# Kernel tuning notes

Measured on AMD Instinct MI355X. Metric: run time of the kernel, lower is better.

The kernel has to match this reference:

```python
import jax, jax.numpy as jnp
import numpy as np

N_NODES = 100000
N_EDGES = 3200000
D_IN = 128
D_HID = 128
N_CLASSES = 2
N_GRAPHS = 64


def _gcn_conv(x, src, dst, norm, W, b, n_nodes):
    # GCNConv: x' = D^-1/2 (A+I) D^-1/2 (x W) + b  (self-loops already in src/dst)
    h = x @ W                                   # [N, out]
    msg = h[src] * norm[:, None]                # gather + per-edge scale [E', out]
    agg = jax.ops.segment_sum(msg, dst, num_segments=n_nodes)  # scatter-add
    return agg + b


def setup_inputs() -> dict:
    key = jax.random.key(0)
    ks = jax.random.split(key, 10)
    x = jax.random.normal(ks[0], (N_NODES, D_IN), dtype=jnp.float32)
    edge_index = jax.random.randint(ks[1], (2, N_EDGES), 0, N_NODES, dtype=jnp.int32)
    batch = jnp.sort(jax.random.randint(ks[2], (N_NODES,), 0, N_GRAPHS, dtype=jnp.int32))
    s1 = 1.0 / np.sqrt(D_IN)
    s2 = 1.0 / np.sqrt(D_HID)
    W1 = jax.random.uniform(ks[3], (D_IN, D_HID), jnp.float32, -s1, s1)
    b1 = jnp.zeros((D_HID,), jnp.float32)
    W2 = jax.random.uniform(ks[4], (D_HID, D_HID), jnp.float32, -s2, s2)
    b2 = jnp.zeros((D_HID,), jnp.float32)
    Wc = jax.random.uniform(ks[5], (D_HID, N_CLASSES), jnp.float32, -s2, s2)
    bc = jnp.zeros((N_CLASSES,), jnp.float32)
    return {"x": x, "edge_index": edge_index, "batch": batch,
            "W1": W1, "b1": b1, "W2": W2, "b2": b2, "Wc": Wc, "bc": bc,
            "num_graphs": N_GRAPHS}


def reference(x, edge_index, batch, W1, b1, W2, b2, Wc, bc, num_graphs):
    n = x.shape[0]
    loops = jnp.arange(n, dtype=edge_index.dtype)
    src = jnp.concatenate([edge_index[0], loops])
    dst = jnp.concatenate([edge_index[1], loops])
    # symmetric normalization with self-loops (degree over destinations, as PyG)
    deg = jax.ops.segment_sum(jnp.ones_like(dst, dtype=x.dtype), dst, num_segments=n)
    dinv = jnp.where(deg > 0, jax.lax.rsqrt(jnp.maximum(deg, 1.0)), 0.0)
    norm = dinv[src] * dinv[dst]                # [E']

    h = _gcn_conv(x, src, dst, norm, W1, b1, n)
    h = jax.nn.relu(h)                          # dropout is identity at eval
    h = _gcn_conv(h, src, dst, norm, W2, b2, n)

    # global_mean_pool over graph ids
    sums = jax.ops.segment_sum(h, batch, num_segments=num_graphs)      # [G, H]
    cnts = jax.ops.segment_sum(jnp.ones((n,), h.dtype), batch, num_segments=num_graphs)
    pooled = sums / jnp.maximum(cnts, 1.0)[:, None]

    return pooled @ Wc + bc                     # [G, num_classes]
```

## Files before the change

### kernel.cpp

```cpp
#include <hip/hip_runtime.h>
#include <hip/hip_bf16.h>

#define D 128
#define NGRAPH 64
#define POOLBLK 256
#define PBCHUNK 4096
#define WINSZ 256
#define WINSLOTS 16384
#define XP 136

typedef __attribute__((ext_vector_type(4))) float f32x4;
typedef __attribute__((ext_vector_type(8))) short bf16x8;

__device__ __forceinline__ unsigned short f2bf(float f) {
    union { float f; unsigned int i; } u; u.f = f;
    unsigned int r = u.i + 0x7fffu + ((u.i >> 16) & 1u);
    return (unsigned short)(r >> 16);
}
__device__ __forceinline__ float2 bf2_to_f2(unsigned int u) {
    union { unsigned int i; float f; } a, b;
    a.i = u << 16;
    b.i = u & 0xffff0000u;
    return make_float2(a.f, b.f);
}


__global__ __launch_bounds__(256) void k_prep(const float* __restrict__ W2,
                                              const float* __restrict__ Wc,
                                              const float* __restrict__ b2,
                                              const float* __restrict__ bc,
                                              float* __restrict__ Weff,
                                              float* __restrict__ beff,
                                              int* __restrict__ zero_region,
                                              int zero_words) {
    int t = threadIdx.x;
    int i = t >> 1, c = t & 1;
    float acc = 0.f;
    for (int k = 0; k < D; ++k) acc += W2[i * D + k] * Wc[k * 2 + c];
    Weff[i * 2 + c] = acc;
    if (i == 0) {
        float s = 0.f;
        for (int k = 0; k < D; ++k) s += b2[k] * Wc[k * 2 + c];
        beff[c] = s + bc[c];
    }
    for (int j = t; j < zero_words; j += 256) zero_region[j] = 0;
}


__global__ __launch_bounds__(256) void k_part(const int* __restrict__ src,
                                              const int* __restrict__ dst,
                                              int* __restrict__ cursor,
                                              unsigned* __restrict__ ebuf,
                                              int E, int nb) {
    __shared__ unsigned spack[PBCHUNK];
    __shared__ unsigned short sbin[PBCHUNK];
    __shared__ unsigned short slrank[PBCHUNK];
    __shared__ int hist[400];
    __shared__ int base[400];
    int tid = threadIdx.x;
    for (int i = tid; i < nb; i += 256) hist[i] = 0;
    __syncthreads();
    int b0 = blockIdx.x * PBCHUNK;
    int cnt = min(PBCHUNK, E - b0);
    for (int j = tid; j < cnt; j += 256) {
        int s = __builtin_nontemporal_load(&src[b0 + j]);
        int d = __builtin_nontemporal_load(&dst[b0 + j]);
        int bin = d >> 8;
        spack[j] = (unsigned)s | ((unsigned)(d & 255) << 17);
        sbin[j] = (unsigned short)bin;
        slrank[j] = (unsigned short)atomicAdd(&hist[bin], 1);
    }
    __syncthreads();
    for (int i = tid; i < nb; i += 256)
        base[i] = hist[i] ? atomicAdd(&cursor[i], hist[i]) : 0;
    __syncthreads();
    for (int j = tid; j < cnt; j += 256) {
        int bin = sbin[j];
        ebuf[(size_t)bin * WINSLOTS + base[bin] + slrank[j]] = spack[j];
    }
}

__global__ __launch_bounds__(256) void k_csrwin(const unsigned* __restrict__ ebuf,
                                                const int* __restrict__ cursor,
                                                int* __restrict__ csr,
                                                int2* __restrict__ offcnt,
                                                float* __restrict__ dinv, int n) {
    __shared__ int hist[WINSZ];
    __shared__ int lscan[WINSZ];
    __shared__ int sexcl[WINSZ];
    int b = blockIdx.x;
    int tid = threadIdx.x;
    hist[tid] = 0;
    __syncthreads();
    int cnt = cursor[b];
    const unsigned* eb = ebuf + (size_t)b * WINSLOTS;
    for (int j = tid; j < cnt; j += 256)
        atomicAdd(&hist[eb[j] >> 17], 1);
    __syncthreads();
    int deg = hist[tid];
    lscan[tid] = deg;
    __syncthreads();
    for (int off = 1; off < 256; off <<= 1) {
        int y = (tid >= off) ? lscan[tid - off] : 0;
        __syncthreads();
        lscan[tid] += y;
        __syncthreads();
    }
    int excl = lscan[tid] - deg;
    int v = b * WINSZ + tid;
    int gbase = b * WINSLOTS;
    if (v < n) {
        offcnt[v] = make_int2(gbase + excl, deg);
        dinv[v] = rsqrtf((float)(deg + 1));
    }
    hist[tid] = 0;
    sexcl[tid] = excl;
    __syncthreads();
    for (int j = tid; j < cnt; j += 256) {
        unsigned p = eb[j];
        int d8 = (int)(p >> 17);
        int lr = atomicAdd(&hist[d8], 1);
        csr[gbase + sexcl[d8] + lr] = (int)(p & 0x1FFFFu);
    }
}


__global__ __launch_bounds__(256) void k_gemm_mfma(const float* __restrict__ X,
                                                   const float* __restrict__ W1,
                                                   unsigned short* __restrict__ H, int nrows) {
    __shared__ unsigned short xs[64][XP];
    __shared__ unsigned short wt[128][XP];
    int tid = threadIdx.x;
    int m0 = blockIdx.x * 64;
    for (int i = tid; i < 2048; i += 256) {
        int elt = i * 8;
        int k = elt >> 7, n0 = elt & 127;
        float4 a = *(const float4*)&W1[k * D + n0];
        float4 b = *(const float4*)&W1[k * D + n0 + 4];
        wt[n0 + 0][k] = f2bf(a.x); wt[n0 + 1][k] = f2bf(a.y);
        wt[n0 + 2][k] = f2bf(a.z); wt[n0 + 3][k] = f2bf(a.w);
        wt[n0 + 4][k] = f2bf(b.x); wt[n0 + 5][k] = f2bf(b.y);
        wt[n0 + 6][k] = f2bf(b.z); wt[n0 + 7][k] = f2bf(b.w);
    }
    for (int i = tid; i < 2048; i += 256) {
        int elt = i * 4;
        int r = elt >> 7, c = elt & 127;
        int gr = m0 + r;
        float4 v = (gr < nrows) ? *(const float4*)&X[(size_t)gr * D + c]
                                : make_float4(0.f, 0.f, 0.f, 0.f);
        ushort4 bv;
        bv.x = f2bf(v.x); bv.y = f2bf(v.y); bv.z = f2bf(v.z); bv.w = f2bf(v.w);
        *(ushort4*)&xs[r][c] = bv;
    }
    __syncthreads();
    int wv = tid >> 6, lane = tid & 63;
    int lrow = lane & 15, lk = (lane >> 4) * 8;
    f32x4 acc[8];
#pragma unroll
    for (int i = 0; i < 8; ++i) acc[i] = (f32x4){0.f, 0.f, 0.f, 0.f};
#pragma unroll
    for (int kk = 0; kk < 128; kk += 32) {
        bf16x8 a = *(bf16x8*)&xs[wv * 16 + lrow][kk + lk];
#pragma unroll
        for (int nt = 0; nt < 8; ++nt) {
            bf16x8 b = *(bf16x8*)&wt[nt * 16 + lrow][kk + lk];
            acc[nt] = __builtin_amdgcn_mfma_f32_16x16x32_bf16(a, b, acc[nt], 0, 0, 0);
        }
    }
    int orow = m0 + wv * 16 + (lane >> 4) * 4;
#pragma unroll
    for (int nt = 0; nt < 8; ++nt) {
#pragma unroll
        for (int r = 0; r < 4; ++r) {
            int gr = orow + r;
            if (gr < nrows) H[(size_t)gr * D + nt * 16 + lrow] = f2bf(acc[nt][r]);
        }
    }
}


__global__ __launch_bounds__(256) void k_agg_proj(const unsigned short* __restrict__ H,
                                                  const int2* __restrict__ offcnt,
                                                  const int* __restrict__ csr,
                                                  const float* __restrict__ dinv,
                                                  const float* __restrict__ bias,
                                                  const float* __restrict__ Weff,
                                                  float2* __restrict__ z, int n) {
    int wid = threadIdx.x >> 6;
    int lane = threadIdx.x & 63;
    int v = blockIdx.x * 4 + wid;
    if (v >= n) return;
    float dv = dinv[v];
    int l2 = lane * 2;
    unsigned us = *(const unsigned*)(H + (size_t)v * D + l2);
    float2 hs = bf2_to_f2(us);
    float dv2 = dv * dv;
    float2 acc = make_float2(hs.x * dv2, hs.y * dv2);
    int2 oc = offcnt[v];
    int e = oc.x, eE = oc.x + oc.y;
    for (; e + 7 < eE; e += 8) {
        int s[8];
#pragma unroll
        for (int j = 0; j < 8; ++j) s[j] = csr[e + j];
        unsigned u[8];
#pragma unroll
        for (int j = 0; j < 8; ++j) u[j] = *(const unsigned*)(H + (size_t)s[j] * D + l2);
        float w[8];
#pragma unroll
        for (int j = 0; j < 8; ++j) w[j] = dinv[s[j]] * dv;
#pragma unroll
        for (int j = 0; j < 8; ++j) {
            float2 h = bf2_to_f2(u[j]);
            acc.x += h.x * w[j]; acc.y += h.y * w[j];
        }
    }
    for (; e + 3 < eE; e += 4) {
        int s0 = csr[e], s1 = csr[e + 1], s2 = csr[e + 2], s3 = csr[e + 3];
        unsigned u0 = *(const unsigned*)(H + (size_t)s0 * D + l2);
        unsigned u1 = *(const unsigned*)(H + (size_t)s1 * D + l2);
        unsigned u2 = *(const unsigned*)(H + (size_t)s2 * D + l2);
        unsigned u3 = *(const unsigned*)(H + (size_t)s3 * D + l2);
        float w0 = dinv[s0] * dv, w1 = dinv[s1] * dv;
        float w2 = dinv[s2] * dv, w3 = dinv[s3] * dv;
        float2 h0 = bf2_to_f2(u0), h1 = bf2_to_f2(u1);
        float2 h2 = bf2_to_f2(u2), h3 = bf2_to_f2(u3);
        acc.x += h0.x * w0; acc.y += h0.y * w0;
        acc.x += h1.x * w1; acc.y += h1.y * w1;
        acc.x += h2.x * w2; acc.y += h2.y * w2;
        acc.x += h3.x * w3; acc.y += h3.y * w3;
    }
    for (; e < eE; ++e) {
        int s0 = csr[e];
        float w0 = dinv[s0] * dv;
        unsigned u0 = *(const unsigned*)(H + (size_t)s0 * D + l2);
        float2 h0 = bf2_to_f2(u0);
        acc.x += h0.x * w0; acc.y += h0.y * w0;
    }
    float2 b = ((const float2*)bias)[lane];
    acc.x = fmaxf(acc.x + b.x, 0.f);
    acc.y = fmaxf(acc.y + b.y, 0.f);
    float4 wv = *(const float4*)&Weff[l2 * 2];
    float z0 = acc.x * wv.x + acc.y * wv.z;
    float z1 = acc.x * wv.y + acc.y * wv.w;
#pragma unroll
    for (int off = 32; off >= 1; off >>= 1) {
        z0 += __shfl_xor(z0, off, 64);
        z1 += __shfl_xor(z1, off, 64);
    }
    if (lane == 0) z[v] = make_float2(z0, z1);
}


__global__ __launch_bounds__(256) void k_pool_edges(const float2* __restrict__ z,
                                                    const int* __restrict__ src,
                                                    const int* __restrict__ dst,
                                                    const float* __restrict__ dinv,
                                                    const int* __restrict__ batch,
                                                    float* __restrict__ tsum,
                                                    int* __restrict__ cnt,
                                                    int n, int E) {
    __shared__ float t[4][NGRAPH * 2];
    __shared__ int scnt[4][NGRAPH];
    int tid = threadIdx.x;
    int wv = tid >> 6;
    for (int j = tid; j < 4 * NGRAPH * 2; j += 256) ((float*)t)[j] = 0.f;
    for (int j = tid; j < 4 * NGRAPH; j += 256) ((int*)scnt)[j] = 0;
    __syncthreads();

    int i = (blockIdx.x * 256 + tid) * 4;
    int stride = POOLBLK * 256 * 4;
    for (; i < E; i += stride) {
        if (i + 3 < E) {
            int4 s4 = *(const int4*)&src[i];
            int4 d4 = *(const int4*)&dst[i];
            float w0 = dinv[s4.x] * dinv[d4.x];
            float w1 = dinv[s4.y] * dinv[d4.y];
            float w2 = dinv[s4.z] * dinv[d4.z];
            float w3 = dinv[s4.w] * dinv[d4.w];
            float2 z0 = z[s4.x], z1 = z[s4.y], z2 = z[s4.z], z3 = z[s4.w];
            int g0 = batch[d4.x], g1 = batch[d4.y], g2 = batch[d4.z], g3 = batch[d4.w];
            atomicAdd(&t[wv][g0 * 2],     w0 * z0.x);
            atomicAdd(&t[wv][g0 * 2 + 1], w0 * z0.y);
            atomicAdd(&t[wv][g1 * 2],     w1 * z1.x);
            atomicAdd(&t[wv][g1 * 2 + 1], w1 * z1.y);
            atomicAdd(&t[wv][g2 * 2],     w2 * z2.x);
            atomicAdd(&t[wv][g2 * 2 + 1], w2 * z2.y);
            atomicAdd(&t[wv][g3 * 2],     w3 * z3.x);
            atomicAdd(&t[wv][g3 * 2 + 1], w3 * z3.y);
        } else {
            for (int j = i; j < E; ++j) {
                int s = src[j], d = dst[j];
                float w = dinv[s] * dinv[d];
                float2 zv = z[s];
                int g = batch[d];
                atomicAdd(&t[wv][g * 2],     w * zv.x);
                atomicAdd(&t[wv][g * 2 + 1], w * zv.y);
            }
        }
    }
    for (int v = blockIdx.x * 256 + tid; v < n; v += POOLBLK * 256) {
        float dv = dinv[v];
        float2 zv = z[v];
        int g = batch[v];
        float w = dv * dv;
        atomicAdd(&t[wv][g * 2],     w * zv.x);
        atomicAdd(&t[wv][g * 2 + 1], w * zv.y);
        atomicAdd(&scnt[wv][g], 1);
    }
    __syncthreads();
    if (tid < NGRAPH * 2) {
        float s = t[0][tid] + t[1][tid] + t[2][tid] + t[3][tid];
        if (s != 0.f) atomicAdd(&tsum[tid], s);
    }
    if (tid < NGRAPH) {
        int s = scnt[0][tid] + scnt[1][tid] + scnt[2][tid] + scnt[3][tid];
        if (s) atomicAdd(&cnt[tid], s);
    }
}

__global__ void k_classify(const float* __restrict__ tsum, const int* __restrict__ cnt,
                           const float* __restrict__ beff, const float* __restrict__ bc,
                           float* __restrict__ out) {
    int t = threadIdx.x;
    if (t >= NGRAPH * 2) return;
    int g = t >> 1, c = t & 1;
    int cg = cnt[g];
    out[t] = cg ? (tsum[t] / (float)cg + beff[c]) : bc[c];
}


extern "C" void kernel_launch(void* const* d_in, const int* in_sizes, int n_in,
                              void* d_out, int out_size, void* d_ws, size_t ws_size,
                              hipStream_t stream) {
    const float* x    = (const float*)d_in[0];
    const int*   ei   = (const int*)d_in[1];
    const int*   batch= (const int*)d_in[2];
    const float* W1   = (const float*)d_in[3];
    const float* b1   = (const float*)d_in[4];
    const float* W2   = (const float*)d_in[5];
    const float* b2   = (const float*)d_in[6];
    const float* Wc   = (const float*)d_in[7];
    const float* bc   = (const float*)d_in[8];

    const int n = in_sizes[0] / D;
    const int E = in_sizes[1] / 2;
    const int* src = ei;
    const int* dst = ei + E;
    const int nb = (n + WINSZ - 1) / WINSZ;

    char* ws = (char*)d_ws;
    size_t off = 0;
    auto carve = [&](size_t bytes) -> char* {
        char* p = ws + off;
        off = (off + bytes + 255) & ~(size_t)255;
        return p;
    };
    unsigned short* bufBF = (unsigned short*)carve((size_t)n * D * 2);
    float2* z     = (float2*)carve((size_t)n * 8);
    unsigned* ebuf= (unsigned*)carve((size_t)nb * WINSLOTS * 4);
    int*   csr    = (int*)  carve((size_t)nb * WINSLOTS * 4);
    const int zero_words = 512 + NGRAPH * 2 + NGRAPH;
    int*   cursor = (int*)  carve(zero_words * 4);
    float* tsum   = (float*)(cursor + 512);
    int*   cnt    = (int*)  (tsum + NGRAPH * 2);
    int2*  offcnt = (int2*) carve((size_t)n * 8);
    float* dinv   = (float*)carve((size_t)n * 4);
    float* Weff   = (float*)carve(D * 2 * 4);
    float* beff   = (float*)carve(2 * 4);

    k_prep<<<1, 256, 0, stream>>>(W2, Wc, b2, bc, Weff, beff, cursor, zero_words);
    k_part<<<(E + PBCHUNK - 1) / PBCHUNK, 256, 0, stream>>>(src, dst, cursor, ebuf, E, nb);
    k_csrwin<<<nb, 256, 0, stream>>>(ebuf, cursor, csr, offcnt, dinv, n);

    k_gemm_mfma<<<(n + 63) / 64, 256, 0, stream>>>(x, W1, bufBF, n);
    k_agg_proj<<<(n + 3) / 4, 256, 0, stream>>>(bufBF, offcnt, csr, dinv, b1, Weff, z, n);

    k_pool_edges<<<POOLBLK, 256, 0, stream>>>(z, src, dst, dinv, batch, tsum, cnt, n, E);
    k_classify<<<1, 128, 0, stream>>>(tsum, cnt, beff, bc, (float*)d_out);
}
```

Baseline: 290.1 us.

## Precompute transposed bf16 W1, double GEMM row tile, slim partition smem

k_prep now also writes a transposed bf16 copy of W1 once, so each GEMM block does plain vector copies into shared memory instead of a strided convert-and-transpose. The GEMM row tile grows from 64 to 128 rows, giving each wave two M-subtiles that reuse the same B fragments, at the cost of more shared memory and registers per block. k_part drops its per-edge shared staging arrays and rereads src/dst in a second pass, ranking edges with a second atomic histogram. Zeroing moves to hipMemsetAsync and the prep kernel runs after CSR construction; edge order within a bin now depends on atomic ordering rather than being fixed.

```diff
diff --git a/kernel.cpp b/kernel.cpp
--- a/kernel.cpp
+++ b/kernel.cpp
@@ -8,6 +8,7 @@
 #define WINSZ 256
 #define WINSLOTS 16384
 #define XP 136
+#define GBM 128
 
 typedef __attribute__((ext_vector_type(4))) float f32x4;
 typedef __attribute__((ext_vector_type(8))) short bf16x8;
@@ -25,25 +26,42 @@
 }
 
 
-__global__ __launch_bounds__(256) void k_prep(const float* __restrict__ W2,
+__global__ __launch_bounds__(256) void k_prep(const float* __restrict__ W1,
+                                              const float* __restrict__ W2,
                                               const float* __restrict__ Wc,
                                               const float* __restrict__ b2,
                                               const float* __restrict__ bc,
                                               float* __restrict__ Weff,
                                               float* __restrict__ beff,
-                                              int* __restrict__ zero_region,
-                                              int zero_words) {
+                                              unsigned short* __restrict__ W1bfT) {
     int t = threadIdx.x;
     int i = t >> 1, c = t & 1;
-    float acc = 0.f;
-    for (int k = 0; k < D; ++k) acc += W2[i * D + k] * Wc[k * 2 + c];
-    Weff[i * 2 + c] = acc;
+    float a0 = 0.f, a1 = 0.f, a2 = 0.f, a3 = 0.f, a4 = 0.f, a5 = 0.f, a6 = 0.f, a7 = 0.f;
+    for (int k = 0; k < D; k += 8) {
+        a0 += W2[i * D + k + 0] * Wc[(k + 0) * 2 + c];
+        a1 += W2[i * D + k + 1] * Wc[(k + 1) * 2 + c];
+        a2 += W2[i * D + k + 2] * Wc[(k + 2) * 2 + c];
+        a3 += W2[i * D + k + 3] * Wc[(k + 3) * 2 + c];
+        a4 += W2[i * D + k + 4] * Wc[(k + 4) * 2 + c];
+        a5 += W2[i * D + k + 5] * Wc[(k + 5) * 2 + c];
+        a6 += W2[i * D + k + 6] * Wc[(k + 6) * 2 + c];
+        a7 += W2[i * D + k + 7] * Wc[(k + 7) * 2 + c];
+    }
+    Weff[i * 2 + c] = ((a0 + a1) + (a2 + a3)) + ((a4 + a5) + (a6 + a7));
     if (i == 0) {
-        float s = 0.f;
-        for (int k = 0; k < D; ++k) s += b2[k] * Wc[k * 2 + c];
-        beff[c] = s + bc[c];
-    }
-    for (int j = t; j < zero_words; j += 256) zero_region[j] = 0;
+        float s0 = 0.f, s1 = 0.f, s2 = 0.f, s3 = 0.f;
+        for (int k = 0; k < D; k += 4) {
+            s0 += b2[k + 0] * Wc[(k + 0) * 2 + c];
+            s1 += b2[k + 1] * Wc[(k + 1) * 2 + c];
+            s2 += b2[k + 2] * Wc[(k + 2) * 2 + c];
+            s3 += b2[k + 3] * Wc[(k + 3) * 2 + c];
+        }
+        beff[c] = (s0 + s1) + (s2 + s3) + bc[c];
+    }
+    for (int e = t; e < D * D; e += 256) {
+        int k = e >> 7, nn = e & 127;
+        W1bfT[nn * D + k] = f2bf(W1[k * D + nn]);
+    }
 }
 
 
@@ -52,31 +70,28 @@
                                               int* __restrict__ cursor,
                                               unsigned* __restrict__ ebuf,
                                               int E, int nb) {
-    __shared__ unsigned spack[PBCHUNK];
-    __shared__ unsigned short sbin[PBCHUNK];
-    __shared__ unsigned short slrank[PBCHUNK];
     __shared__ int hist[400];
+    __shared__ int hist2[400];
     __shared__ int base[400];
     int tid = threadIdx.x;
-    for (int i = tid; i < nb; i += 256) hist[i] = 0;
+    for (int i = tid; i < nb; i += 256) { hist[i] = 0; hist2[i] = 0; }
     __syncthreads();
     int b0 = blockIdx.x * PBCHUNK;
     int cnt = min(PBCHUNK, E - b0);
     for (int j = tid; j < cnt; j += 256) {
-        int s = __builtin_nontemporal_load(&src[b0 + j]);
         int d = __builtin_nontemporal_load(&dst[b0 + j]);
-        int bin = d >> 8;
-        spack[j] = (unsigned)s | ((unsigned)(d & 255) << 17);
-        sbin[j] = (unsigned short)bin;
-        slrank[j] = (unsigned short)atomicAdd(&hist[bin], 1);
+        atomicAdd(&hist[d >> 8], 1);
     }
     __syncthreads();
     for (int i = tid; i < nb; i += 256)
         base[i] = hist[i] ? atomicAdd(&cursor[i], hist[i]) : 0;
     __syncthreads();
     for (int j = tid; j < cnt; j += 256) {
-        int bin = sbin[j];
-        ebuf[(size_t)bin * WINSLOTS + base[bin] + slrank[j]] = spack[j];
+        int s = src[b0 + j];
+        int d = dst[b0 + j];
+        int bin = d >> 8;
+        int pos = base[bin] + atomicAdd(&hist2[bin], 1);
+        ebuf[(size_t)bin * WINSLOTS + pos] = (unsigned)s | ((unsigned)(d & 255) << 17);
     }
 }
 
@@ -126,54 +141,62 @@
 
 
 __global__ __launch_bounds__(256) void k_gemm_mfma(const float* __restrict__ X,
-                                                   const float* __restrict__ W1,
+                                                   const unsigned short* __restrict__ W1bfT,
                                                    unsigned short* __restrict__ H, int nrows) {
-    __shared__ unsigned short xs[64][XP];
+    __shared__ unsigned short xs[GBM][XP];
     __shared__ unsigned short wt[128][XP];
     int tid = threadIdx.x;
-    int m0 = blockIdx.x * 64;
-    for (int i = tid; i < 2048; i += 256) {
-        int elt = i * 8;
-        int k = elt >> 7, n0 = elt & 127;
-        float4 a = *(const float4*)&W1[k * D + n0];
-        float4 b = *(const float4*)&W1[k * D + n0 + 4];
-        wt[n0 + 0][k] = f2bf(a.x); wt[n0 + 1][k] = f2bf(a.y);
-        wt[n0 + 2][k] = f2bf(a.z); wt[n0 + 3][k] = f2bf(a.w);
-        wt[n0 + 4][k] = f2bf(b.x); wt[n0 + 5][k] = f2bf(b.y);
-        wt[n0 + 6][k] = f2bf(b.z); wt[n0 + 7][k] = f2bf(b.w);
-    }
-    for (int i = tid; i < 2048; i += 256) {
-        int elt = i * 4;
-        int r = elt >> 7, c = elt & 127;
-        int gr = m0 + r;
-        float4 v = (gr < nrows) ? *(const float4*)&X[(size_t)gr * D + c]
-                                : make_float4(0.f, 0.f, 0.f, 0.f);
-        ushort4 bv;
-        bv.x = f2bf(v.x); bv.y = f2bf(v.y); bv.z = f2bf(v.z); bv.w = f2bf(v.w);
-        *(ushort4*)&xs[r][c] = bv;
+    int m0 = blockIdx.x * GBM;
+    {
+        const uint4* wsrc = (const uint4*)W1bfT;
+        for (int i = tid; i < 2048; i += 256) {
+            uint4 v = wsrc[i];
+            int elt = i * 8;
+            int r = elt >> 7, c = elt & 127;
+            *(uint4*)&wt[r][c] = v;
+        }
+    }
+    {
+        for (int i = tid; i < 4096; i += 256) {
+            int elt = i * 4;
+            int r = elt >> 7, c = elt & 127;
+            int gr = m0 + r;
+            float4 v = (gr < nrows) ? *(const float4*)&X[(size_t)gr * D + c]
+                                    : make_float4(0.f, 0.f, 0.f, 0.f);
+            ushort4 bv;
+            bv.x = f2bf(v.x); bv.y = f2bf(v.y); bv.z = f2bf(v.z); bv.w = f2bf(v.w);
+            *(ushort4*)&xs[r][c] = bv;
+        }
     }
     __syncthreads();
     int wv = tid >> 6, lane = tid & 63;
     int lrow = lane & 15, lk = (lane >> 4) * 8;
-    f32x4 acc[8];
-#pragma unroll
-    for (int i = 0; i < 8; ++i) acc[i] = (f32x4){0.f, 0.f, 0.f, 0.f};
+    f32x4 acc[2][8];
+#pragma unroll
+    for (int mt = 0; mt < 2; ++mt)
+#pragma unroll
+        for (int i = 0; i < 8; ++i) acc[mt][i] = (f32x4){0.f, 0.f, 0.f, 0.f};
 #pragma unroll
     for (int kk = 0; kk < 128; kk += 32) {
-        bf16x8 a = *(bf16x8*)&xs[wv * 16 + lrow][kk + lk];
+        bf16x8 a0 = *(bf16x8*)&xs[wv * 32 + lrow][kk + lk];
+        bf16x8 a1 = *(bf16x8*)&xs[wv * 32 + 16 + lrow][kk + lk];
 #pragma unroll
         for (int nt = 0; nt < 8; ++nt) {
             bf16x8 b = *(bf16x8*)&wt[nt * 16 + lrow][kk + lk];
-            acc[nt] = __builtin_amdgcn_mfma_f32_16x16x32_bf16(a, b, acc[nt], 0, 0, 0);
-        }
-    }
-    int orow = m0 + wv * 16 + (lane >> 4) * 4;
-#pragma unroll
-    for (int nt = 0; nt < 8; ++nt) {
-#pragma unroll
-        for (int r = 0; r < 4; ++r) {
-            int gr = orow + r;
-            if (gr < nrows) H[(size_t)gr * D + nt * 16 + lrow] = f2bf(acc[nt][r]);
+            acc[0][nt] = __builtin_amdgcn_mfma_f32_16x16x32_bf16(a0, b, acc[0][nt], 0, 0, 0);
+            acc[1][nt] = __builtin_amdgcn_mfma_f32_16x16x32_bf16(a1, b, acc[1][nt], 0, 0, 0);
+        }
+    }
+#pragma unroll
+    for (int mt = 0; mt < 2; ++mt) {
+        int orow = m0 + wv * 32 + mt * 16 + (lane >> 4) * 4;
+#pragma unroll
+        for (int nt = 0; nt < 8; ++nt) {
+#pragma unroll
+            for (int r = 0; r < 4; ++r) {
+                int gr = orow + r;
+                if (gr < nrows) H[(size_t)gr * D + nt * 16 + lrow] = f2bf(acc[mt][nt][r]);
+            }
         }
     }
 }
@@ -367,12 +390,15 @@
     float* dinv   = (float*)carve((size_t)n * 4);
     float* Weff   = (float*)carve(D * 2 * 4);
     float* beff   = (float*)carve(2 * 4);
-
-    k_prep<<<1, 256, 0, stream>>>(W2, Wc, b2, bc, Weff, beff, cursor, zero_words);
+    unsigned short* W1bfT = (unsigned short*)carve(D * D * 2);
+
+    hipMemsetAsync(cursor, 0, zero_words * 4, stream);
+
     k_part<<<(E + PBCHUNK - 1) / PBCHUNK, 256, 0, stream>>>(src, dst, cursor, ebuf, E, nb);
     k_csrwin<<<nb, 256, 0, stream>>>(ebuf, cursor, csr, offcnt, dinv, n);
-
-    k_gemm_mfma<<<(n + 63) / 64, 256, 0, stream>>>(x, W1, bufBF, n);
+    k_prep<<<1, 256, 0, stream>>>(W1, W2, Wc, b2, bc, Weff, beff, W1bfT);
+
+    k_gemm_mfma<<<(n + GBM - 1) / GBM, 256, 0, stream>>>(x, W1bfT, bufBF, n);
     k_agg_proj<<<(n + 3) / 4, 256, 0, stream>>>(bufBF, offcnt, csr, dinv, b1, Weff, z, n);
 
     k_pool_edges<<<POOLBLK, 256, 0, stream>>>(z, src, dst, dinv, batch, tsum, cnt, n, E);
```

Result: slower. 328.5 us (+13.2%).
